# Performance work log

Hardware: AMD Instinct MI355X
Metric: run time of the kernel (lower is better)

Reference implementation:

```python
import jax, jax.numpy as jnp
import numpy as np

# --- Instant-NGP hash-grid constants (from __init__ defaults) ---
T = 2 ** 19          # hash table size per level
NLEVELS = 16
F = 2                # features per level
L = 4                # dir positional-encoding frequencies
LEVELS = np.geomspace(16, 2048, NLEVELS, dtype=int)            # grid resolutions
PRIMES = jnp.array([1, 2654435761, 805459861], dtype=jnp.uint32)
FREQS = (2.0 ** np.arange(L)).astype(np.float32)
# corner c in 0..7 -> bit b_i = use ceil along dim i (matches torch corner order)
BITS = jnp.array([[(c >> i) & 1 for i in range(3)] for c in range(8)], dtype=bool)  # (8,3)


def _hash_encode(pos, table):
    """pos: (P,3) level-scaled positions; table: (T,F). Returns (P,F).
    Spatial hash + gather + trilinear interpolation (== grid_sample trick)."""
    fl = jnp.floor(pos)
    ce = jnp.ceil(pos)
    frac = pos - fl                                             # (P,3) in [0,1)
    corners = jnp.where(BITS[None], ce[:, None, :], fl[:, None, :]).astype(jnp.int32)  # (P,8,3)
    # uint32 wrap-around arithmetic matches torch int64 mod 2^19 (T is a power of 2)
    v = corners.astype(jnp.uint32) * PRIMES                     # (P,8,3)
    h = (v[..., 0] ^ v[..., 1] ^ v[..., 2]) & jnp.uint32(T - 1) # (P,8)
    cf = table[h]                                               # (P,8,F) irregular gather
    w = jnp.prod(jnp.where(BITS[None], frac[:, None, :], 1.0 - frac[:, None, :]), axis=-1)  # (P,8)
    return jnp.einsum('pc,pcf->pf', w, cf)


def setup_inputs() -> dict:
    key = jax.random.key(0)
    ks = jax.random.split(key, 16)
    N, S = 2048, 192
    # positions s.t. x*scene_scale + 0.5 lies mostly in (0,1), a few outside (mask path)
    x = (jax.random.uniform(ks[0], (N, S, 3), jnp.float32) - 0.5) * 1.1
    r_dir = jax.random.normal(ks[1], (N, S, 3), jnp.float32)
    tables = jax.random.normal(ks[2], (NLEVELS, T, F), jnp.float32) * 1e-4

    def lin(k, fan_in, fan_out):
        return jax.random.normal(k, (fan_in, fan_out), jnp.float32) / np.float32(np.sqrt(fan_in))

    din = F * NLEVELS              # 32
    cin = 16 + 3 + 3 * L * 2       # 43
    return {
        'x': x, 'r_dir': r_dir, 'tables': tables,
        'dW1': lin(ks[3], din, 64), 'db1': jnp.zeros((64,), jnp.float32),
        'dW2': lin(ks[4], 64, 16), 'db2': jnp.zeros((16,), jnp.float32),
        'cW1': lin(ks[5], cin, 64), 'cb1': jnp.zeros((64,), jnp.float32),
        'cW2': lin(ks[6], 64, 64), 'cb2': jnp.zeros((64,), jnp.float32),
        'cW3': lin(ks[7], 64, 3), 'cb3': jnp.zeros((3,), jnp.float32),
    }


def reference(x, r_dir, tables, dW1, db1, dW2, db2, cW1, cb1, cW2, cb2, cW3, cb3):
    scene_scale = 1.0
    N, S = x.shape[0], r_dir.shape[1]
    xf = x.reshape(-1, 3) * scene_scale + 0.5          # (P,3)
    rd = r_dir.reshape(-1, 3)                          # (P,3)
    mask = jnp.all(xf > 0, axis=-1) & jnp.all(xf < 1, axis=-1)  # (P,)

    # multi-resolution hash encoding (fixed 16-level loop, vectorized over points)
    feats = jnp.concatenate(
        [_hash_encode(xf * np.float32(LEVELS[i]), tables[i]) for i in range(NLEVELS)],
        axis=-1)                                       # (P, F*NLEVELS)

    log_sigma = jax.nn.relu(feats @ dW1 + db1) @ dW2 + db2        # (P,16)

    # direction positional encoding: [dir, sin(2^l*2pi*dir), cos(...)] -> (P, 3+3*2L)
    xin = rd[..., None] * (2.0 * np.pi * jnp.asarray(FREQS))      # (P,3,L)
    enc = jnp.concatenate([jnp.sin(xin), jnp.cos(xin)], axis=-1).reshape(rd.shape[0], -1)
    enc_dir = jnp.concatenate([rd, enc], axis=-1)                 # (P,27)

    h = jax.nn.relu(jnp.concatenate([log_sigma, enc_dir], axis=-1) @ cW1 + cb1)
    h = jax.nn.relu(h @ cW2 + cb2)
    color = jax.nn.sigmoid(h @ cW3 + cb3)                         # (P,3)

    color = jnp.where(mask[:, None], color, 0.0)
    sigma = jnp.where(mask[:, None], jnp.exp(log_sigma[:, :1]), 0.0)
    return color.reshape(N, S, 3), sigma.reshape(N, S, 1)
```

## Files before the change

### kernel.cpp

```cpp
#include <hip/hip_runtime.h>
#include <hip/hip_bf16.h>
#include <cstdint>

#define NPTS (2048 * 192)
#define TBL  (1u << 19)
#define TMASK (TBL - 1u)
#define PBLOCKS (NPTS / 256)
#define ENC_BLOCKS (PBLOCKS * 16)
#define PREP_BLOCKS 6
#define MLP_BLOCKS 768
#define P2 2654435761u
#define P3 805459861u

__constant__ float LVLS[16] = {16.f, 22.f, 30.f, 42.f, 58.f, 80.f, 111.f, 153.f,
                               212.f, 294.f, 406.f, 561.f, 776.f, 1072.f, 1482.f, 2048.f};

__device__ __forceinline__ uint32_t f2bf(float f) {
    uint32_t u = __float_as_uint(f);
    return (u + 0x7FFFu + ((u >> 16) & 1u)) >> 16;
}
__device__ __forceinline__ uint32_t pack2(float a, float b) {
    return f2bf(a) | (f2bf(b) << 16);
}

#if __has_builtin(__builtin_amdgcn_sinf)
#define SIN_REV(x) __builtin_amdgcn_sinf(x)
#define COS_REV(x) __builtin_amdgcn_cosf(x)
#else
#define SIN_REV(x) __sinf(6.28318530717958647f * (x))
#define COS_REV(x) __cosf(6.28318530717958647f * (x))
#endif

typedef __attribute__((ext_vector_type(8))) short bf16x8;
typedef __attribute__((ext_vector_type(4))) float f32x4;

#define MFMA_BF16 __builtin_amdgcn_mfma_f32_16x16x32_bf16

__global__ __launch_bounds__(256) void k_encode(const float* __restrict__ x,
                                                const float* __restrict__ tables,
                                                uint32_t* __restrict__ feats,
                                                const float* __restrict__ dW1,
                                                const float* __restrict__ dW2,
                                                const float* __restrict__ cW1,
                                                const float* __restrict__ cb1,
                                                const float* __restrict__ cW2,
                                                const float* __restrict__ cW3,
                                                uint4* __restrict__ wfrags)
{
    if (blockIdx.x >= ENC_BLOCKS) {
        int t = (blockIdx.x - ENC_BLOCKS) * 256 + threadIdx.x;
        if (t >= 24 * 64) return;
        int frag = t >> 6, lane = t & 63;
        const float* W; const float* bfold = nullptr;
        int OUT, Kact, Mact, k0, m0;
        if (frag < 4)       { W = dW1; OUT = 64; Kact = 32; Mact = 64; k0 = 0;               m0 = frag * 16; }
        else if (frag < 6)  { W = dW2; OUT = 16; Kact = 64; Mact = 16; k0 = (frag - 4) * 32; m0 = 0; }
        else if (frag < 14) { int i = frag - 6;  W = cW1; OUT = 64; Kact = 43; Mact = 64;
                              k0 = (i & 1) * 32; m0 = (i >> 1) * 16; bfold = cb1; }
        else if (frag < 22) { int i = frag - 14; W = cW2; OUT = 64; Kact = 64; Mact = 64;
                              k0 = (i & 1) * 32; m0 = (i >> 1) * 16; }
        else                { W = cW3; OUT = 3;  Kact = 64; Mact = 3;  k0 = (frag - 22) * 32; m0 = 0; }
        int m  = m0 + (lane & 15);
        int kq = k0 + ((lane >> 4) << 3);
        uint32_t d[4];
#pragma unroll
        for (int j = 0; j < 4; ++j) {
            float a0 = 0.f, a1 = 0.f;
            int ka = kq + 2 * j, kb = ka + 1;
            if (m < Mact) {
                a0 = (ka < Kact) ? W[(size_t)ka * OUT + m]
                                 : ((bfold && ka == Kact) ? bfold[m] : 0.f);
                a1 = (kb < Kact) ? W[(size_t)kb * OUT + m]
                                 : ((bfold && kb == Kact) ? bfold[m] : 0.f);
            }
            d[j] = f2bf(a0) | (f2bf(a1) << 16);
        }
        wfrags[t] = make_uint4(d[0], d[1], d[2], d[3]);
        return;
    }

    int xs   = blockIdx.x & 7;
    int i    = blockIdx.x >> 3;
    int half = i / PBLOCKS;
    int pb   = i - half * PBLOCKS;
    int lvl  = xs + (half << 3);
    int p    = pb * 256 + threadIdx.x;

    size_t p3 = (size_t)p * 3;
    float x0 = x[p3 + 0] + 0.5f;
    float x1 = x[p3 + 1] + 0.5f;
    float x2 = x[p3 + 2] + 0.5f;
    size_t oidx = (size_t)lvl * NPTS + p;

    bool m = (x0 > 0.f) && (x0 < 1.f) && (x1 > 0.f) && (x1 < 1.f) &&
             (x2 > 0.f) && (x2 < 1.f);
    if (!m) { feats[oidx] = 0u; return; }

    float s  = LVLS[lvl];
    float px = x0 * s, py = x1 * s, pz = x2 * s;
    float flx = floorf(px), fly = floorf(py), flz = floorf(pz);
    float frx = px - flx,   fry = py - fly,   frz = pz - flz;
    int ix = (int)flx, iy = (int)fly, iz = (int)flz;
    uint32_t ux = (uint32_t)ix, uy = (uint32_t)iy, uz = (uint32_t)iz;

    uint32_t base[4];
    base[0] = (uy * P2) ^ (uz * P3);
    base[1] = ((uy + 1u) * P2) ^ (uz * P3);
    base[2] = (uy * P2) ^ ((uz + 1u) * P3);
    base[3] = ((uy + 1u) * P2) ^ ((uz + 1u) * P3);

    const float2* tb = (const float2*)tables + (size_t)lvl * TBL;

    float2 v[8];
    if ((ix & 1) == 0) {
        const float4* tb4 = (const float4*)tb;
#pragma unroll
        for (int cc = 0; cc < 4; ++cc) {
            uint32_t h0 = (base[cc] ^ ux) & TMASK;
            float4 qv = tb4[h0 >> 1];
            bool hi = (h0 & 1u) != 0u;
            float2 e0 = hi ? make_float2(qv.z, qv.w) : make_float2(qv.x, qv.y);
            float2 e1 = hi ? make_float2(qv.x, qv.y) : make_float2(qv.z, qv.w);
            v[(cc << 1)]     = e0;
            v[(cc << 1) | 1] = e1;
        }
    } else {
        uint32_t h[8];
#pragma unroll
        for (int c = 0; c < 8; ++c)
            h[c] = (base[c >> 1] ^ (ux + (uint32_t)(c & 1))) & TMASK;
#pragma unroll
        for (int c = 0; c < 8; ++c) v[c] = tb[h[c]];
    }

    float f0 = 0.f, f1 = 0.f;
#pragma unroll
    for (int c = 0; c < 8; ++c) {
        float w = ((c & 1)        ? frx : 1.f - frx)
                * (((c >> 1) & 1) ? fry : 1.f - fry)
                * (((c >> 2) & 1) ? frz : 1.f - frz);
        f0 += w * v[c].x;
        f1 += w * v[c].y;
    }
    feats[oidx] = pack2(f0, f1);
}

__device__ __forceinline__ bf16x8 trans_frag(uint32_t p01a, uint32_t p23a,
                                             uint32_t p01b, uint32_t p23b, int lane)
{
    int q = lane >> 4, col = lane & 15;
    int srcA = (((q & 1) << 1) << 4) | col;
    int srcB = srcA + 16;
    uint32_t a0 = (uint32_t)__shfl((int)p01a, srcA, 64);
    uint32_t b0 = (uint32_t)__shfl((int)p01b, srcA, 64);
    uint32_t a1 = (uint32_t)__shfl((int)p23a, srcA, 64);
    uint32_t b1 = (uint32_t)__shfl((int)p23b, srcA, 64);
    uint32_t a2 = (uint32_t)__shfl((int)p01a, srcB, 64);
    uint32_t b2 = (uint32_t)__shfl((int)p01b, srcB, 64);
    uint32_t a3 = (uint32_t)__shfl((int)p23a, srcB, 64);
    uint32_t b3 = (uint32_t)__shfl((int)p23b, srcB, 64);
    bool hi = q >= 2;
    union { bf16x8 v; uint32_t d[4]; } u;
    u.d[0] = hi ? b0 : a0;
    u.d[1] = hi ? b1 : a1;
    u.d[2] = hi ? b2 : a2;
    u.d[3] = hi ? b3 : a3;
    return u.v;
}

__device__ __forceinline__ float pe_val(int r, float rx, float ry, float rz)
{
    int t = r - 19;
    int d = t >> 3;
    int s = t & 7;
    float comp = (d == 0) ? rx : ((d == 1) ? ry : rz);
    float a  = ldexpf(comp, s & 3);
    float sv = SIN_REV(a);
    float cv = COS_REV(a);
    float v  = (s < 4) ? sv : cv;
    if (r == 16) v = rx;
    if (r == 17) v = ry;
    if (r == 18) v = rz;
    if (r == 43) v = 1.0f;
    if (r > 43)  v = 0.0f;
    return v;
}

__global__ __launch_bounds__(256) void k_mlp(const uint32_t* __restrict__ feats,
                                             const uint4* __restrict__ wfrags,
                                             const float* __restrict__ x,
                                             const float* __restrict__ rdir,
                                             const float* __restrict__ db1,
                                             const float* __restrict__ db2,
                                             const float* __restrict__ cb2,
                                             const float* __restrict__ cb3,
                                             float* __restrict__ out)
{
    int lane = threadIdx.x & 63;
    int q = lane >> 4, col = lane & 15;
    int wgid = blockIdx.x * 4 + (threadIdx.x >> 6);

    union { bf16x8 v; uint4 u; } wf;
    bf16x8 A1[4], A2[2], A3[4][2], A4[4][2], A5[2];
#pragma unroll
    for (int mt = 0; mt < 4; ++mt) { wf.u = wfrags[(0 + mt) * 64 + lane]; A1[mt] = wf.v; }
#pragma unroll
    for (int kt = 0; kt < 2; ++kt) { wf.u = wfrags[(4 + kt) * 64 + lane]; A2[kt] = wf.v; }
#pragma unroll
    for (int mt = 0; mt < 4; ++mt)
#pragma unroll
        for (int kt = 0; kt < 2; ++kt) {
            wf.u = wfrags[(6 + 2 * mt + kt) * 64 + lane];  A3[mt][kt] = wf.v;
            wf.u = wfrags[(14 + 2 * mt + kt) * 64 + lane]; A4[mt][kt] = wf.v;
        }
#pragma unroll
    for (int kt = 0; kt < 2; ++kt) { wf.u = wfrags[(22 + kt) * 64 + lane]; A5[kt] = wf.v; }

    for (int it = 0; it < 8; ++it) {
        int g = (wgid * 8 + it) << 4;
        int pt = g + col;
        size_t pt3 = (size_t)pt * 3;

        union { bf16x8 v; uint32_t d[4]; } Bf;
#pragma unroll
        for (int w = 0; w < 4; ++w)
            Bf.d[w] = feats[(size_t)(q * 4 + w) * NPTS + g + col];

        f32x4 T[4];
#pragma unroll
        for (int mt = 0; mt < 4; ++mt) {
            const float4 bb = *(const float4*)&db1[mt * 16 + q * 4];
            f32x4 c; c[0] = bb.x; c[1] = bb.y; c[2] = bb.z; c[3] = bb.w;
            T[mt] = MFMA_BF16(A1[mt], Bf.v, c, 0, 0, 0);
        }
        uint32_t p01[4], p23[4];
#pragma unroll
        for (int mt = 0; mt < 4; ++mt) {
            p01[mt] = pack2(fmaxf(T[mt][0], 0.f), fmaxf(T[mt][1], 0.f));
            p23[mt] = pack2(fmaxf(T[mt][2], 0.f), fmaxf(T[mt][3], 0.f));
        }
        bf16x8 Bh0 = trans_frag(p01[0], p23[0], p01[1], p23[1], lane);
        bf16x8 Bh1 = trans_frag(p01[2], p23[2], p01[3], p23[3], lane);

        f32x4 Dls;
        {
            const float4 bb = *(const float4*)&db2[q * 4];
            f32x4 c; c[0] = bb.x; c[1] = bb.y; c[2] = bb.z; c[3] = bb.w;
            Dls = MFMA_BF16(A2[0], Bh0, c, 0, 0, 0);
            Dls = MFMA_BF16(A2[1], Bh1, Dls, 0, 0, 0);
        }
        uint32_t lp01 = pack2(Dls[0], Dls[1]);
        uint32_t lp23 = pack2(Dls[2], Dls[3]);

        float rx = rdir[pt3 + 0], ry = rdir[pt3 + 1], rz = rdir[pt3 + 2];

        union { bf16x8 v; uint32_t d[4]; } Ba0, Ba1;
        Ba0.v = trans_frag(lp01, lp23, lp01, lp23, lane);
        {
            int base = q << 3;
#pragma unroll
            for (int j = 0; j < 4; ++j) {
                uint32_t pk = pack2(pe_val(base + 2 * j, rx, ry, rz),
                                    pe_val(base + 2 * j + 1, rx, ry, rz));
                if (q >= 2) Ba0.d[j] = pk;
            }
        }
        {
            int base = 32 + (q << 3);
#pragma unroll
            for (int j = 0; j < 4; ++j)
                Ba1.d[j] = pack2(pe_val(base + 2 * j, rx, ry, rz),
                                 pe_val(base + 2 * j + 1, rx, ry, rz));
        }

        f32x4 C1[4];
#pragma unroll
        for (int mt = 0; mt < 4; ++mt) {
            f32x4 c = {0.f, 0.f, 0.f, 0.f};
            c = MFMA_BF16(A3[mt][0], Ba0.v, c, 0, 0, 0);
            C1[mt] = MFMA_BF16(A3[mt][1], Ba1.v, c, 0, 0, 0);
        }
#pragma unroll
        for (int mt = 0; mt < 4; ++mt) {
            p01[mt] = pack2(fmaxf(C1[mt][0], 0.f), fmaxf(C1[mt][1], 0.f));
            p23[mt] = pack2(fmaxf(C1[mt][2], 0.f), fmaxf(C1[mt][3], 0.f));
        }
        bf16x8 Bc0 = trans_frag(p01[0], p23[0], p01[1], p23[1], lane);
        bf16x8 Bc1 = trans_frag(p01[2], p23[2], p01[3], p23[3], lane);

        f32x4 C2[4];
#pragma unroll
        for (int mt = 0; mt < 4; ++mt) {
            const float4 bb = *(const float4*)&cb2[mt * 16 + q * 4];
            f32x4 c; c[0] = bb.x; c[1] = bb.y; c[2] = bb.z; c[3] = bb.w;
            c = MFMA_BF16(A4[mt][0], Bc0, c, 0, 0, 0);
            C2[mt] = MFMA_BF16(A4[mt][1], Bc1, c, 0, 0, 0);
        }
#pragma unroll
        for (int mt = 0; mt < 4; ++mt) {
            p01[mt] = pack2(fmaxf(C2[mt][0], 0.f), fmaxf(C2[mt][1], 0.f));
            p23[mt] = pack2(fmaxf(C2[mt][2], 0.f), fmaxf(C2[mt][3], 0.f));
        }
        bf16x8 Bd0 = trans_frag(p01[0], p23[0], p01[1], p23[1], lane);
        bf16x8 Bd1 = trans_frag(p01[2], p23[2], p01[3], p23[3], lane);

        f32x4 c5 = {0.f, 0.f, 0.f, 0.f};
        if (q == 0) { c5[0] = cb3[0]; c5[1] = cb3[1]; c5[2] = cb3[2]; }
        f32x4 Dc = MFMA_BF16(A5[0], Bd0, c5, 0, 0, 0);
        Dc = MFMA_BF16(A5[1], Bd1, Dc, 0, 0, 0);

        if (q == 0) {
            float xfx = x[pt3 + 0] + 0.5f;
            float xfy = x[pt3 + 1] + 0.5f;
            float xfz = x[pt3 + 2] + 0.5f;
            bool m = (xfx > 0.f) && (xfx < 1.f) && (xfy > 0.f) && (xfy < 1.f) &&
                     (xfz > 0.f) && (xfz < 1.f);
            out[pt3 + 0] = m ? 1.f / (1.f + __expf(-Dc[0])) : 0.f;
            out[pt3 + 1] = m ? 1.f / (1.f + __expf(-Dc[1])) : 0.f;
            out[pt3 + 2] = m ? 1.f / (1.f + __expf(-Dc[2])) : 0.f;
            out[(size_t)3 * NPTS + pt] = m ? __expf(Dls[0]) : 0.f;
        }
    }
}

extern "C" void kernel_launch(void* const* d_in, const int* in_sizes, int n_in,
                              void* d_out, int out_size, void* d_ws, size_t ws_size,
                              hipStream_t stream) {
    const float* x      = (const float*)d_in[0];
    const float* rdir   = (const float*)d_in[1];
    const float* tables = (const float*)d_in[2];
    const float* dW1 = (const float*)d_in[3];
    const float* db1 = (const float*)d_in[4];
    const float* dW2 = (const float*)d_in[5];
    const float* db2 = (const float*)d_in[6];
    const float* cW1 = (const float*)d_in[7];
    const float* cb1 = (const float*)d_in[8];
    const float* cW2 = (const float*)d_in[9];
    const float* cb2 = (const float*)d_in[10];
    const float* cW3 = (const float*)d_in[11];
    const float* cb3 = (const float*)d_in[12];
    float* out = (float*)d_out;

    uint4*    wfrags = (uint4*)d_ws;
    uint32_t* feats  = (uint32_t*)((char*)d_ws + 32768);

    k_encode<<<ENC_BLOCKS + PREP_BLOCKS, 256, 0, stream>>>(
        x, tables, feats, dW1, dW2, cW1, cb1, cW2, cW3, wfrags);
    k_mlp<<<MLP_BLOCKS, 256, 0, stream>>>(feats, wfrags, x, rdir,
                                          db1, db2, cb2, cb3, out);
}
```

Measured before the change: 256.9 us.

## Switch MLP to fp16 16x16x16 MFMA so outputs chain without lane shuffles

```diff
diff --git a/kernel.cpp b/kernel.cpp
--- a/kernel.cpp
+++ b/kernel.cpp
@@ -7,7 +7,7 @@
 #define TMASK (TBL - 1u)
 #define PBLOCKS (NPTS / 256)
 #define ENC_BLOCKS (PBLOCKS * 16)
-#define PREP_BLOCKS 6
+#define PREP_BLOCKS 11
 #define MLP_BLOCKS 768
 #define P2 2654435761u
 #define P3 805459861u
@@ -15,26 +15,33 @@
 __constant__ float LVLS[16] = {16.f, 22.f, 30.f, 42.f, 58.f, 80.f, 111.f, 153.f,
                                212.f, 294.f, 406.f, 561.f, 776.f, 1072.f, 1482.f, 2048.f};
 
-__device__ __forceinline__ uint32_t f2bf(float f) {
-    uint32_t u = __float_as_uint(f);
-    return (u + 0x7FFFu + ((u >> 16) & 1u)) >> 16;
-}
-__device__ __forceinline__ uint32_t pack2(float a, float b) {
-    return f2bf(a) | (f2bf(b) << 16);
-}
-
 #if __has_builtin(__builtin_amdgcn_sinf)
 #define SIN_REV(x) __builtin_amdgcn_sinf(x)
-#define COS_REV(x) __builtin_amdgcn_cosf(x)
 #else
 #define SIN_REV(x) __sinf(6.28318530717958647f * (x))
-#define COS_REV(x) __cosf(6.28318530717958647f * (x))
 #endif
 
-typedef __attribute__((ext_vector_type(8))) short bf16x8;
-typedef __attribute__((ext_vector_type(4))) float f32x4;
-
-#define MFMA_BF16 __builtin_amdgcn_mfma_f32_16x16x32_bf16
+typedef __fp16 h16x2 __attribute__((ext_vector_type(2)));
+typedef __fp16 h16x4 __attribute__((ext_vector_type(4)));
+typedef float  f32x4 __attribute__((ext_vector_type(4)));
+
+#if __has_builtin(__builtin_amdgcn_mfma_f32_16x16x16_f16)
+#define MFMA16(A, B, C) __builtin_amdgcn_mfma_f32_16x16x16_f16(A, B, C, 0, 0, 0)
+#else
+#define MFMA16(A, B, C) __builtin_amdgcn_mfma_f32_16x16x16f16(A, B, C, 0, 0, 0)
+#endif
+
+__device__ __forceinline__ uint32_t pkh(float a, float b) {
+#if __has_builtin(__builtin_amdgcn_cvt_pkrtz)
+    union { h16x2 h; uint32_t u; } t;
+    t.h = __builtin_amdgcn_cvt_pkrtz(a, b);
+    return t.u;
+#else
+    union { __fp16 e[2]; uint32_t u; } t;
+    t.e[0] = (__fp16)a; t.e[1] = (__fp16)b;
+    return t.u;
+#endif
+}
 
 __global__ __launch_bounds__(256) void k_encode(const float* __restrict__ x,
                                                 const float* __restrict__ tables,
@@ -45,37 +52,36 @@
                                                 const float* __restrict__ cb1,
                                                 const float* __restrict__ cW2,
                                                 const float* __restrict__ cW3,
-                                                uint4* __restrict__ wfrags)
+                                                uint2* __restrict__ wfrags)
 {
     if (blockIdx.x >= ENC_BLOCKS) {
         int t = (blockIdx.x - ENC_BLOCKS) * 256 + threadIdx.x;
-        if (t >= 24 * 64) return;
+        if (t >= 44 * 64) return;
         int frag = t >> 6, lane = t & 63;
+        int q = lane >> 4, col = lane & 15;
         const float* W; const float* bfold = nullptr;
         int OUT, Kact, Mact, k0, m0;
-        if (frag < 4)       { W = dW1; OUT = 64; Kact = 32; Mact = 64; k0 = 0;               m0 = frag * 16; }
-        else if (frag < 6)  { W = dW2; OUT = 16; Kact = 64; Mact = 16; k0 = (frag - 4) * 32; m0 = 0; }
-        else if (frag < 14) { int i = frag - 6;  W = cW1; OUT = 64; Kact = 43; Mact = 64;
-                              k0 = (i & 1) * 32; m0 = (i >> 1) * 16; bfold = cb1; }
-        else if (frag < 22) { int i = frag - 14; W = cW2; OUT = 64; Kact = 64; Mact = 64;
-                              k0 = (i & 1) * 32; m0 = (i >> 1) * 16; }
-        else                { W = cW3; OUT = 3;  Kact = 64; Mact = 3;  k0 = (frag - 22) * 32; m0 = 0; }
-        int m  = m0 + (lane & 15);
-        int kq = k0 + ((lane >> 4) << 3);
-        uint32_t d[4];
+        if (frag < 8)       { int i = frag;      W = dW1; OUT = 64; Kact = 32; Mact = 64;
+                              k0 = (i & 1) * 16; m0 = (i >> 1) * 16; }
+        else if (frag < 12) { W = dW2; OUT = 16; Kact = 64; Mact = 16; k0 = (frag - 8) * 16; m0 = 0; }
+        else if (frag < 24) { int i = frag - 12; W = cW1; OUT = 64; Kact = 43; Mact = 64;
+                              k0 = (i % 3) * 16; m0 = (i / 3) * 16; bfold = cb1; }
+        else if (frag < 40) { int i = frag - 24; W = cW2; OUT = 64; Kact = 64; Mact = 64;
+                              k0 = (i & 3) * 16; m0 = (i >> 2) * 16; }
+        else                { W = cW3; OUT = 3;  Kact = 64; Mact = 3;  k0 = (frag - 40) * 16; m0 = 0; }
+        int m = m0 + col;
+        union { __fp16 e[4]; uint2 u; } o;
 #pragma unroll
         for (int j = 0; j < 4; ++j) {
-            float a0 = 0.f, a1 = 0.f;
-            int ka = kq + 2 * j, kb = ka + 1;
+            int k = k0 + q * 4 + j;
+            float v = 0.f;
             if (m < Mact) {
-                a0 = (ka < Kact) ? W[(size_t)ka * OUT + m]
-                                 : ((bfold && ka == Kact) ? bfold[m] : 0.f);
-                a1 = (kb < Kact) ? W[(size_t)kb * OUT + m]
-                                 : ((bfold && kb == Kact) ? bfold[m] : 0.f);
+                if (k < Kact) v = W[(size_t)k * OUT + m];
+                else if (bfold && k == Kact) v = bfold[m];
             }
-            d[j] = f2bf(a0) | (f2bf(a1) << 16);
-        }
-        wfrags[t] = make_uint4(d[0], d[1], d[2], d[3]);
+            o.e[j] = (__fp16)v;
+        }
+        wfrags[t] = o.u;
         return;
     }
 
@@ -142,30 +148,7 @@
         f0 += w * v[c].x;
         f1 += w * v[c].y;
     }
-    feats[oidx] = pack2(f0, f1);
-}
-
-__device__ __forceinline__ bf16x8 trans_frag(uint32_t p01a, uint32_t p23a,
-                                             uint32_t p01b, uint32_t p23b, int lane)
-{
-    int q = lane >> 4, col = lane & 15;
-    int srcA = (((q & 1) << 1) << 4) | col;
-    int srcB = srcA + 16;
-    uint32_t a0 = (uint32_t)__shfl((int)p01a, srcA, 64);
-    uint32_t b0 = (uint32_t)__shfl((int)p01b, srcA, 64);
-    uint32_t a1 = (uint32_t)__shfl((int)p23a, srcA, 64);
-    uint32_t b1 = (uint32_t)__shfl((int)p23b, srcA, 64);
-    uint32_t a2 = (uint32_t)__shfl((int)p01a, srcB, 64);
-    uint32_t b2 = (uint32_t)__shfl((int)p01b, srcB, 64);
-    uint32_t a3 = (uint32_t)__shfl((int)p23a, srcB, 64);
-    uint32_t b3 = (uint32_t)__shfl((int)p23b, srcB, 64);
-    bool hi = q >= 2;
-    union { bf16x8 v; uint32_t d[4]; } u;
-    u.d[0] = hi ? b0 : a0;
-    u.d[1] = hi ? b1 : a1;
-    u.d[2] = hi ? b2 : a2;
-    u.d[3] = hi ? b3 : a3;
-    return u.v;
+    feats[oidx] = pkh(f0, f1);
 }
 
 __device__ __forceinline__ float pe_val(int r, float rx, float ry, float rz)
@@ -174,10 +157,8 @@
     int d = t >> 3;
     int s = t & 7;
     float comp = (d == 0) ? rx : ((d == 1) ? ry : rz);
-    float a  = ldexpf(comp, s & 3);
-    float sv = SIN_REV(a);
-    float cv = COS_REV(a);
-    float v  = (s < 4) ? sv : cv;
+    float a = ldexpf(comp, s & 3) + ((s >= 4) ? 0.25f : 0.0f);
+    float v = SIN_REV(a);
     if (r == 16) v = rx;
     if (r == 17) v = ry;
     if (r == 18) v = rz;
@@ -187,7 +168,7 @@
 }
 
 __global__ __launch_bounds__(256) void k_mlp(const uint32_t* __restrict__ feats,
-                                             const uint4* __restrict__ wfrags,
+                                             const uint2* __restrict__ wfrags,
                                              const float* __restrict__ x,
                                              const float* __restrict__ rdir,
                                              const float* __restrict__ db1,
@@ -200,114 +181,101 @@
     int q = lane >> 4, col = lane & 15;
     int wgid = blockIdx.x * 4 + (threadIdx.x >> 6);
 
-    union { bf16x8 v; uint4 u; } wf;
-    bf16x8 A1[4], A2[2], A3[4][2], A4[4][2], A5[2];
-#pragma unroll
-    for (int mt = 0; mt < 4; ++mt) { wf.u = wfrags[(0 + mt) * 64 + lane]; A1[mt] = wf.v; }
-#pragma unroll
-    for (int kt = 0; kt < 2; ++kt) { wf.u = wfrags[(4 + kt) * 64 + lane]; A2[kt] = wf.v; }
+    union Fr { h16x4 v; uint2 u; uint32_t d[2]; };
+
+    Fr A1[4][2], A2[4], A3[4][3], A4[4][4], A5[4];
 #pragma unroll
     for (int mt = 0; mt < 4; ++mt)
 #pragma unroll
-        for (int kt = 0; kt < 2; ++kt) {
-            wf.u = wfrags[(6 + 2 * mt + kt) * 64 + lane];  A3[mt][kt] = wf.v;
-            wf.u = wfrags[(14 + 2 * mt + kt) * 64 + lane]; A4[mt][kt] = wf.v;
-        }
-#pragma unroll
-    for (int kt = 0; kt < 2; ++kt) { wf.u = wfrags[(22 + kt) * 64 + lane]; A5[kt] = wf.v; }
+        for (int kt = 0; kt < 2; ++kt) A1[mt][kt].u = wfrags[(mt * 2 + kt) * 64 + lane];
+#pragma unroll
+    for (int kt = 0; kt < 4; ++kt) A2[kt].u = wfrags[(8 + kt) * 64 + lane];
+#pragma unroll
+    for (int mt = 0; mt < 4; ++mt)
+#pragma unroll
+        for (int kt = 0; kt < 3; ++kt) A3[mt][kt].u = wfrags[(12 + mt * 3 + kt) * 64 + lane];
+#pragma unroll
+    for (int mt = 0; mt < 4; ++mt)
+#pragma unroll
+        for (int kt = 0; kt < 4; ++kt) A4[mt][kt].u = wfrags[(24 + mt * 4 + kt) * 64 + lane];
+#pragma unroll
+    for (int kt = 0; kt < 4; ++kt) A5[kt].u = wfrags[(40 + kt) * 64 + lane];
 
     for (int it = 0; it < 8; ++it) {
         int g = (wgid * 8 + it) << 4;
         int pt = g + col;
         size_t pt3 = (size_t)pt * 3;
 
-        union { bf16x8 v; uint32_t d[4]; } Bf;
-#pragma unroll
-        for (int w = 0; w < 4; ++w)
-            Bf.d[w] = feats[(size_t)(q * 4 + w) * NPTS + g + col];
-
-        f32x4 T[4];
+        Fr Bf0, Bf1;
+        Bf0.d[0] = feats[(size_t)(2 * q + 0) * NPTS + pt];
+        Bf0.d[1] = feats[(size_t)(2 * q + 1) * NPTS + pt];
+        Bf1.d[0] = feats[(size_t)(8 + 2 * q + 0) * NPTS + pt];
+        Bf1.d[1] = feats[(size_t)(8 + 2 * q + 1) * NPTS + pt];
+
+        f32x4 D1[4];
 #pragma unroll
         for (int mt = 0; mt < 4; ++mt) {
             const float4 bb = *(const float4*)&db1[mt * 16 + q * 4];
             f32x4 c; c[0] = bb.x; c[1] = bb.y; c[2] = bb.z; c[3] = bb.w;
-            T[mt] = MFMA_BF16(A1[mt], Bf.v, c, 0, 0, 0);
-        }
-        uint32_t p01[4], p23[4];
+            c = MFMA16(A1[mt][0].v, Bf0.v, c);
+            D1[mt] = MFMA16(A1[mt][1].v, Bf1.v, c);
+        }
+        Fr B2[4];
 #pragma unroll
         for (int mt = 0; mt < 4; ++mt) {
-            p01[mt] = pack2(fmaxf(T[mt][0], 0.f), fmaxf(T[mt][1], 0.f));
-            p23[mt] = pack2(fmaxf(T[mt][2], 0.f), fmaxf(T[mt][3], 0.f));
-        }
-        bf16x8 Bh0 = trans_frag(p01[0], p23[0], p01[1], p23[1], lane);
-        bf16x8 Bh1 = trans_frag(p01[2], p23[2], p01[3], p23[3], lane);
+            B2[mt].d[0] = pkh(fmaxf(D1[mt][0], 0.f), fmaxf(D1[mt][1], 0.f));
+            B2[mt].d[1] = pkh(fmaxf(D1[mt][2], 0.f), fmaxf(D1[mt][3], 0.f));
+        }
 
         f32x4 Dls;
         {
             const float4 bb = *(const float4*)&db2[q * 4];
             f32x4 c; c[0] = bb.x; c[1] = bb.y; c[2] = bb.z; c[3] = bb.w;
-            Dls = MFMA_BF16(A2[0], Bh0, c, 0, 0, 0);
-            Dls = MFMA_BF16(A2[1], Bh1, Dls, 0, 0, 0);
-        }
-        uint32_t lp01 = pack2(Dls[0], Dls[1]);
-        uint32_t lp23 = pack2(Dls[2], Dls[3]);
+#pragma unroll
+            for (int kt = 0; kt < 4; ++kt) c = MFMA16(A2[kt].v, B2[kt].v, c);
+            Dls = c;
+        }
 
         float rx = rdir[pt3 + 0], ry = rdir[pt3 + 1], rz = rdir[pt3 + 2];
-
-        union { bf16x8 v; uint32_t d[4]; } Ba0, Ba1;
-        Ba0.v = trans_frag(lp01, lp23, lp01, lp23, lane);
+        Fr B3[3];
+        B3[0].d[0] = pkh(Dls[0], Dls[1]);
+        B3[0].d[1] = pkh(Dls[2], Dls[3]);
         {
-            int base = q << 3;
-#pragma unroll
-            for (int j = 0; j < 4; ++j) {
-                uint32_t pk = pack2(pe_val(base + 2 * j, rx, ry, rz),
-                                    pe_val(base + 2 * j + 1, rx, ry, rz));
-                if (q >= 2) Ba0.d[j] = pk;
-            }
+            int b = 16 + 4 * q;
+            B3[1].d[0] = pkh(pe_val(b + 0, rx, ry, rz), pe_val(b + 1, rx, ry, rz));
+            B3[1].d[1] = pkh(pe_val(b + 2, rx, ry, rz), pe_val(b + 3, rx, ry, rz));
         }
         {
-            int base = 32 + (q << 3);
-#pragma unroll
-            for (int j = 0; j < 4; ++j)
-                Ba1.d[j] = pack2(pe_val(base + 2 * j, rx, ry, rz),
-                                 pe_val(base + 2 * j + 1, rx, ry, rz));
-        }
-
-        f32x4 C1[4];
+            int b = 32 + 4 * q;
+            B3[2].d[0] = pkh(pe_val(b + 0, rx, ry, rz), pe_val(b + 1, rx, ry, rz));
+            B3[2].d[1] = pkh(pe_val(b + 2, rx, ry, rz), pe_val(b + 3, rx, ry, rz));
+        }
+
+        Fr B4[4];
 #pragma unroll
         for (int mt = 0; mt < 4; ++mt) {
             f32x4 c = {0.f, 0.f, 0.f, 0.f};
-            c = MFMA_BF16(A3[mt][0], Ba0.v, c, 0, 0, 0);
-            C1[mt] = MFMA_BF16(A3[mt][1], Ba1.v, c, 0, 0, 0);
-        }
-#pragma unroll
-        for (int mt = 0; mt < 4; ++mt) {
-            p01[mt] = pack2(fmaxf(C1[mt][0], 0.f), fmaxf(C1[mt][1], 0.f));
-            p23[mt] = pack2(fmaxf(C1[mt][2], 0.f), fmaxf(C1[mt][3], 0.f));
-        }
-        bf16x8 Bc0 = trans_frag(p01[0], p23[0], p01[1], p23[1], lane);
-        bf16x8 Bc1 = trans_frag(p01[2], p23[2], p01[3], p23[3], lane);
-
-        f32x4 C2[4];
+#pragma unroll
+            for (int kt = 0; kt < 3; ++kt) c = MFMA16(A3[mt][kt].v, B3[kt].v, c);
+            B4[mt].d[0] = pkh(fmaxf(c[0], 0.f), fmaxf(c[1], 0.f));
+            B4[mt].d[1] = pkh(fmaxf(c[2], 0.f), fmaxf(c[3], 0.f));
+        }
+
+        Fr B5[4];
 #pragma unroll
         for (int mt = 0; mt < 4; ++mt) {
             const float4 bb = *(const float4*)&cb2[mt * 16 + q * 4];
             f32x4 c; c[0] = bb.x; c[1] = bb.y; c[2] = bb.z; c[3] = bb.w;
-            c = MFMA_BF16(A4[mt][0], Bc0, c, 0, 0, 0);
-            C2[mt] = MFMA_BF16(A4[mt][1], Bc1, c, 0, 0, 0);
-        }
-#pragma unroll
-        for (int mt = 0; mt < 4; ++mt) {
-            p01[mt] = pack2(fmaxf(C2[mt][0], 0.f), fmaxf(C2[mt][1], 0.f));
-            p23[mt] = pack2(fmaxf(C2[mt][2], 0.f), fmaxf(C2[mt][3], 0.f));
-        }
-        bf16x8 Bd0 = trans_frag(p01[0], p23[0], p01[1], p23[1], lane);
-        bf16x8 Bd1 = trans_frag(p01[2], p23[2], p01[3], p23[3], lane);
+#pragma unroll
+            for (int kt = 0; kt < 4; ++kt) c = MFMA16(A4[mt][kt].v, B4[kt].v, c);
+            B5[mt].d[0] = pkh(fmaxf(c[0], 0.f), fmaxf(c[1], 0.f));
+            B5[mt].d[1] = pkh(fmaxf(c[2], 0.f), fmaxf(c[3], 0.f));
+        }
 
         f32x4 c5 = {0.f, 0.f, 0.f, 0.f};
         if (q == 0) { c5[0] = cb3[0]; c5[1] = cb3[1]; c5[2] = cb3[2]; }
-        f32x4 Dc = MFMA_BF16(A5[0], Bd0, c5, 0, 0, 0);
-        Dc = MFMA_BF16(A5[1], Bd1, Dc, 0, 0, 0);
+#pragma unroll
+        for (int kt = 0; kt < 4; ++kt) c5 = MFMA16(A5[kt].v, B5[kt].v, c5);
 
         if (q == 0) {
             float xfx = x[pt3 + 0] + 0.5f;
@@ -315,9 +283,9 @@
             float xfz = x[pt3 + 2] + 0.5f;
             bool m = (xfx > 0.f) && (xfx < 1.f) && (xfy > 0.f) && (xfy < 1.f) &&
                      (xfz > 0.f) && (xfz < 1.f);
-            out[pt3 + 0] = m ? 1.f / (1.f + __expf(-Dc[0])) : 0.f;
-            out[pt3 + 1] = m ? 1.f / (1.f + __expf(-Dc[1])) : 0.f;
-            out[pt3 + 2] = m ? 1.f / (1.f + __expf(-Dc[2])) : 0.f;
+            out[pt3 + 0] = m ? 1.f / (1.f + __expf(-c5[0])) : 0.f;
+            out[pt3 + 1] = m ? 1.f / (1.f + __expf(-c5[1])) : 0.f;
+            out[pt3 + 2] = m ? 1.f / (1.f + __expf(-c5[2])) : 0.f;
             out[(size_t)3 * NPTS + pt] = m ? __expf(Dls[0]) : 0.f;
         }
     }
@@ -341,7 +309,7 @@
     const float* cb3 = (const float*)d_in[12];
     float* out = (float*)d_out;
 
-    uint4*    wfrags = (uint4*)d_ws;
+    uint2*    wfrags = (uint2*)d_ws;
     uint32_t* feats  = (uint32_t*)((char*)d_ws + 32768);
 
     k_encode<<<ENC_BLOCKS + PREP_BLOCKS, 256, 0, stream>>>(
```

New measurement: 252.6 us. Within noise of the previous version (-1.7%).
